# Kernel tuning notes

Hardware: AMD Instinct MI355X
Metric: run time of the kernel (lower is better)

Reference implementation:

```python
import jax, jax.numpy as jnp
import numpy as np

N_NODES = 50000
N_EDGES = 800000
F_IN = 128
HEADS = 4
C_OUT = 32
NEG_SLOPE = 0.2
BN_EPS = 1e-5


def _add_self_loops(edge_index, edge_attr, n):
    # PyG fill_value='mean': self-loop attr = mean of incoming edge attrs per node (0 if none)
    src, dst = edge_index[0], edge_index[1]
    deg = jax.ops.segment_sum(jnp.ones_like(edge_attr[:, 0]), dst, num_segments=n)
    loop_attr = jax.ops.segment_sum(edge_attr, dst, num_segments=n) / jnp.maximum(deg, 1.0)[:, None]
    loop = jnp.arange(n)
    src2 = jnp.concatenate([src, loop])
    dst2 = jnp.concatenate([dst, loop])
    attr2 = jnp.concatenate([edge_attr, loop_attr], axis=0)
    return src2, dst2, attr2


def _segment_softmax(logits, seg, n):
    m = jax.ops.segment_max(logits, seg, num_segments=n)
    m = jnp.where(jnp.isfinite(m), m, 0.0)
    ex = jnp.exp(logits - m[seg])
    s = jax.ops.segment_sum(ex, seg, num_segments=n)
    return ex / s[seg]


def _gatv2(x, src, dst, eattr, Wl, bl, Wr, br, We, att, bias, n):
    # x: [n, F]; returns [n, HEADS*C_OUT]
    xl = (x @ Wl + bl).reshape(n, HEADS, C_OUT)
    xr = (x @ Wr + br).reshape(n, HEADS, C_OUT)
    ea = (eattr @ We).reshape(-1, HEADS, C_OUT)
    xlj = xl[src]                                   # [E, H, C] gather
    msg = jax.nn.leaky_relu(xlj + xr[dst] + ea, NEG_SLOPE)
    logits = jnp.einsum('ehc,hc->eh', msg, att)     # [E, H]
    alpha = _segment_softmax(logits, dst, n)
    out = jax.ops.segment_sum(xlj * alpha[..., None], dst, num_segments=n)
    return out.reshape(n, HEADS * C_OUT) + bias


def _batchnorm(x, gamma, beta):
    mu = x.mean(axis=0)
    var = x.var(axis=0)
    return gamma * (x - mu) * jax.lax.rsqrt(var + BN_EPS) + beta


def setup_inputs() -> dict:
    key = jax.random.key(0)
    ks = jax.random.split(key, 20)
    HC = HEADS * C_OUT
    s = 0.05
    inp = {
        'emb': jax.random.normal(ks[0], (N_NODES, F_IN), dtype=jnp.float32),
        'edge_index': jax.random.randint(ks[1], (2, N_EDGES), 0, N_NODES, dtype=jnp.int64),
        'edge_weight': jax.random.uniform(ks[2], (N_EDGES, 1), dtype=jnp.float32),
        'Wl1': jax.random.normal(ks[3], (F_IN, HC)) * s,
        'bl1': jnp.zeros((HC,), jnp.float32),
        'Wr1': jax.random.normal(ks[4], (F_IN, HC)) * s,
        'br1': jnp.zeros((HC,), jnp.float32),
        'We1': jax.random.normal(ks[5], (1, HC)) * s,
        'att1': jax.random.normal(ks[6], (HEADS, C_OUT)) * s,
        'bias1': jnp.zeros((HC,), jnp.float32),
        'gamma1': jnp.ones((HC,), jnp.float32),
        'beta1': jnp.zeros((HC,), jnp.float32),
        'Wl2': jax.random.normal(ks[7], (HC, HC)) * s,
        'bl2': jnp.zeros((HC,), jnp.float32),
        'Wr2': jax.random.normal(ks[8], (HC, HC)) * s,
        'br2': jnp.zeros((HC,), jnp.float32),
        'We2': jax.random.normal(ks[9], (1, HC)) * s,
        'att2': jax.random.normal(ks[10], (HEADS, C_OUT)) * s,
        'bias2': jnp.zeros((HC,), jnp.float32),
    }
    return inp


def reference(emb, edge_index, edge_weight, Wl1, bl1, Wr1, br1, We1, att1, bias1,
              gamma1, beta1, Wl2, bl2, Wr2, br2, We2, att2, bias2):
    n = emb.shape[0]
    src, dst, eattr = _add_self_loops(edge_index, edge_weight, n)
    h1 = _gatv2(emb, src, dst, eattr, Wl1, bl1, Wr1, br1, We1, att1, bias1, n)
    h1 = jax.nn.elu(_batchnorm(h1, gamma1, beta1))
    h2 = _gatv2(h1, src, dst, eattr, Wl2, bl2, Wr2, br2, We2, att2, bias2, n)
    # fusion: mean over [input_emb, h1, h2] along stacked axis
    return (emb + h1 + h2) / 3.0
```

## Files before the change

kernel.cpp:

```cpp
#include <hip/hip_runtime.h>
#include <hip/hip_bf16.h>
#include <math.h>

#define N_NODES 50000
#define N_EDGES 800000
#define HC 128
#define SLOT 64

#define BM 128
#define NBX ((N_NODES + BM - 1) / BM)
#define NCHK 64
#define EPB (N_EDGES / NCHK)
#define NRNG 4
#define RNG_N (N_NODES / NRNG)
#define RNG_W (RNG_N / 2)
#define NW (N_NODES / 2)
#define NSCAT (NCHK * NRNG)
#define NB2 ((NW + 255) / 256)

typedef short bh8 __attribute__((ext_vector_type(8)));
typedef float f4 __attribute__((ext_vector_type(4)));
typedef float f2 __attribute__((ext_vector_type(2)));

__device__ __forceinline__ unsigned int pk2(float a, float b) {
  return (unsigned int)__bfloat16_as_ushort(__float2bfloat16(a)) |
         ((unsigned int)__bfloat16_as_ushort(__float2bfloat16(b)) << 16);
}
__device__ __forceinline__ float blo(unsigned int u) { return __uint_as_float(u << 16); }
__device__ __forceinline__ float bhi(unsigned int u) { return __uint_as_float(u & 0xffff0000u); }
__device__ __forceinline__ f2 vmax2(f2 a, f2 b) {
#if __has_builtin(__builtin_elementwise_max)
  return __builtin_elementwise_max(a, b);
#else
  f2 r; r.x = fmaxf(a.x, b.x); r.y = fmaxf(a.y, b.y); return r;
#endif
}

__global__ __launch_bounds__(256) void k_histprep(
    const float* __restrict__ Wl1, const float* __restrict__ Wr1,
    const float* __restrict__ Wl2, const float* __restrict__ Wr2,
    unsigned short* __restrict__ WtAll,
    float* __restrict__ chsum, float* __restrict__ chsq,
    const int* __restrict__ ei, unsigned int* __restrict__ counts32,
    int* __restrict__ done) {
  __shared__ unsigned int hist[RNG_W];
  int tid = threadIdx.x, bid = blockIdx.x;
  int gid = bid * 256 + tid;
  {
    int m = gid >> 14;
    int idx = gid & 16383;
    const float* src = (m == 0) ? Wl1 : (m == 1) ? Wr1 : (m == 2) ? Wl2 : Wr2;
    int k = idx >> 7, n = idx & 127;
    WtAll[((size_t)m * HC + n) * HC + k] =
        __bfloat16_as_ushort(__float2bfloat16(src[k * HC + n]));
    if (gid < HC) { chsum[gid] = 0.f; chsq[gid] = 0.f; }
    if (gid == 256) *done = 0;
  }
  int c = bid >> 2, r = bid & 3;
  int rb = r * RNG_N;
  for (int w = tid; w < RNG_W; w += 256) hist[w] = 0u;
  __syncthreads();
  const int* dstp = ei + N_EDGES + c * EPB;
  for (int g = tid; g < EPB / 4; g += 256) {
    int4 d4 = *(const int4*)(dstp + g * 4);
    int dl;
    dl = d4.x - rb; if ((unsigned)dl < RNG_N) atomicAdd(&hist[dl >> 1], (dl & 1) ? 0x10000u : 1u);
    dl = d4.y - rb; if ((unsigned)dl < RNG_N) atomicAdd(&hist[dl >> 1], (dl & 1) ? 0x10000u : 1u);
    dl = d4.z - rb; if ((unsigned)dl < RNG_N) atomicAdd(&hist[dl >> 1], (dl & 1) ? 0x10000u : 1u);
    dl = d4.w - rb; if ((unsigned)dl < RNG_N) atomicAdd(&hist[dl >> 1], (dl & 1) ? 0x10000u : 1u);
  }
  __syncthreads();
  unsigned int* dst = counts32 + (size_t)c * NW + r * RNG_W;
  for (int w = tid; w < RNG_W; w += 256) dst[w] = hist[w];
}

__global__ __launch_bounds__(256) void k_scan(const unsigned int* __restrict__ counts32,
                                              unsigned int* __restrict__ bases32,
                                              int* __restrict__ cursor,
                                              int* __restrict__ counts2,
                                              int* __restrict__ bases2,
                                              int* __restrict__ done) {
  __shared__ int dh[80];
  int tid = threadIdx.x;
  int w = blockIdx.x * 256 + tid;
  if (tid < 80) dh[tid] = 0;
  __syncthreads();
  if (w < NW) {
    unsigned int a0 = 0, a1 = 0;
#pragma unroll 4
    for (int b = 0; b < NCHK; ++b) {
      unsigned int v = counts32[(size_t)b * NW + w];
      bases32[(size_t)b * NW + w] = a0 | (a1 << 16);
      a0 += v & 0xffffu;
      a1 += v >> 16;
    }
    cursor[2 * w] = (int)a0;
    cursor[2 * w + 1] = (int)a1;
    atomicAdd(&dh[min((int)a0, SLOT)], 1);
    atomicAdd(&dh[min((int)a1, SLOT)], 1);
  }
  __syncthreads();
  if (tid <= SLOT) counts2[blockIdx.x * 72 + tid] = dh[tid];
  __threadfence();
  __shared__ int ticket;
  if (tid == 0) ticket = atomicAdd(done, 1);
  __syncthreads();
  if (ticket == NB2 - 1) {
    __threadfence();
    __shared__ int colsum[80], cbase[80];
    if (tid <= SLOT) {
      int s = 0;
      for (int b = 0; b < NB2; ++b) s += counts2[b * 72 + tid];
      colsum[tid] = s;
    }
    __syncthreads();
    if (tid == 0) {
      int a = 0;
      for (int i = 0; i <= SLOT; ++i) { cbase[i] = a; a += colsum[i]; }
    }
    __syncthreads();
    if (tid <= SLOT) {
      int a = cbase[tid];
      for (int b = 0; b < NB2; ++b) { bases2[b * 72 + tid] = a; a += counts2[b * 72 + tid]; }
    }
  }
}

__global__ __launch_bounds__(256) void k_scat_g1(
    const int* __restrict__ ei, const float* __restrict__ ew,
    const unsigned int* __restrict__ bases32, unsigned int* __restrict__ slots,
    const float* __restrict__ X, const unsigned short* __restrict__ Wt,
    const float* __restrict__ b0, const float* __restrict__ b1,
    unsigned short* __restrict__ Y0b, float* __restrict__ Y1,
    const int* __restrict__ cursor, const int* __restrict__ bases2,
    int* __restrict__ perm) {
  __shared__ __align__(16) unsigned int lsbuf[16384];
  int tid = threadIdx.x, bid = blockIdx.x;
  if (bid >= NSCAT + NBX) {
    int b2 = bid - NSCAT - NBX;
    int* dcur = (int*)lsbuf;
    if (tid <= SLOT) dcur[tid] = bases2[b2 * 72 + tid];
    __syncthreads();
    for (int i = tid; i < 512; i += 256) {
      int nn = b2 * 512 + i;
      if (nn < N_NODES) {
        int d = min(cursor[nn], SLOT);
        int pos = atomicAdd(&dcur[d], 1);
        perm[pos] = nn;
      }
    }
    return;
  }
  if (bid < NSCAT) {
    int c = bid >> 2, r = bid & 3;
    int rb = r * RNG_N;
    const unsigned int* bp = bases32 + (size_t)c * NW + r * RNG_W;
    for (int w = tid; w < RNG_W; w += 256) lsbuf[w] = bp[w];
    __syncthreads();
    const int* sp = ei + c * EPB;
    const int* dp = ei + N_EDGES + c * EPB;
    const float* wp = ew + c * EPB;
    for (int g = tid; g < EPB / 4; g += 256) {
      int4 s4 = *(const int4*)(sp + g * 4);
      int4 d4 = *(const int4*)(dp + g * 4);
      float4 w4 = *(const float4*)(wp + g * 4);
      int ss[4] = {s4.x, s4.y, s4.z, s4.w};
      int dd[4] = {d4.x, d4.y, d4.z, d4.w};
      float ww[4] = {w4.x, w4.y, w4.z, w4.w};
#pragma unroll
      for (int i = 0; i < 4; ++i) {
        int dl = dd[i] - rb;
        if ((unsigned)dl < RNG_N) {
          unsigned int old = atomicAdd(&lsbuf[dl >> 1], (dl & 1) ? 0x10000u : 1u);
          unsigned int pos = (dl & 1) ? (old >> 16) : (old & 0xffffu);
          unsigned int wq = min((unsigned int)(ww[i] * 65536.f + 0.5f), 65535u);
          if (pos < SLOT)
            slots[(size_t)dd[i] * SLOT + pos] = ((unsigned int)ss[i] << 16) | wq;
        }
      }
    }
    return;
  }
  unsigned short* Xls = (unsigned short*)lsbuf;
  unsigned short* Wls = Xls + 128 * 128;
  int row0 = (bid - NSCAT) * BM;
  {
    int r = tid >> 1;
    int ks = (tid & 1) * 64;
    int gr = row0 + r;
    const float* xp = X + (size_t)gr * HC + ks;
    int sw = r & 15;
#pragma unroll
    for (int i = 0; i < 4; ++i) {
      float f[16];
      if (gr < N_NODES) {
        *(float4*)&f[0] = *(const float4*)(xp + i * 16);
        *(float4*)&f[4] = *(const float4*)(xp + i * 16 + 4);
        *(float4*)&f[8] = *(const float4*)(xp + i * 16 + 8);
        *(float4*)&f[12] = *(const float4*)(xp + i * 16 + 12);
      } else {
#pragma unroll
        for (int j = 0; j < 16; ++j) f[j] = 0.f;
      }
      int kg = (ks >> 3) + i * 2;
      *(uint4*)&Xls[r * 128 + ((kg ^ sw) * 8)] =
          make_uint4(pk2(f[0], f[1]), pk2(f[2], f[3]), pk2(f[4], f[5]), pk2(f[6], f[7]));
      *(uint4*)&Xls[r * 128 + (((kg + 1) ^ sw) * 8)] =
          make_uint4(pk2(f[8], f[9]), pk2(f[10], f[11]), pk2(f[12], f[13]), pk2(f[14], f[15]));
    }
  }
  int lane = tid & 63;
  int wv = tid >> 6;
  int lrow = lane & 15;
  int lq = lane >> 4;
  int rbase = wv * 32;
#pragma unroll
  for (int half = 0; half < 2; ++half) {
    if (half) __syncthreads();
    {
      int n = tid >> 1;
      int ks2 = (tid & 1) * 64;
      const unsigned short* wp = Wt + half * (HC * HC) + n * HC + ks2;
      int swn = n & 15;
#pragma unroll
      for (int g = 0; g < 8; ++g) {
        uint4 v = *(const uint4*)(wp + g * 8);
        int kg = (ks2 >> 3) + g;
        *(uint4*)&Wls[n * 128 + ((kg ^ swn) * 8)] = v;
      }
    }
    __syncthreads();
    f4 acc[2][8];
#pragma unroll
    for (int mt = 0; mt < 2; ++mt)
#pragma unroll
      for (int nt = 0; nt < 8; ++nt) acc[mt][nt] = (f4){0.f, 0.f, 0.f, 0.f};
#pragma unroll
    for (int kk = 0; kk < 4; ++kk) {
      int kg = kk * 4 + lq;
      bh8 a0 = *(const bh8*)&Xls[(rbase + lrow) * 128 + ((kg ^ lrow) * 8)];
      bh8 a1 = *(const bh8*)&Xls[(rbase + 16 + lrow) * 128 + ((kg ^ lrow) * 8)];
#pragma unroll
      for (int nt = 0; nt < 8; ++nt) {
        bh8 b = *(const bh8*)&Wls[(nt * 16 + lrow) * 128 + ((kg ^ lrow) * 8)];
        acc[0][nt] = __builtin_amdgcn_mfma_f32_16x16x32_bf16(a0, b, acc[0][nt], 0, 0, 0);
        acc[1][nt] = __builtin_amdgcn_mfma_f32_16x16x32_bf16(a1, b, acc[1][nt], 0, 0, 0);
      }
    }
    const float* bb = half ? b1 : b0;
    float bv[8];
#pragma unroll
    for (int nt = 0; nt < 8; ++nt) bv[nt] = bb[nt * 16 + lrow];
#pragma unroll
    for (int mt = 0; mt < 2; ++mt) {
#pragma unroll
      for (int rr = 0; rr < 4; ++rr) {
        int gr = row0 + rbase + mt * 16 + lq * 4 + rr;
        if (gr < N_NODES) {
          if (half == 0) {
#pragma unroll
            for (int nt = 0; nt < 8; ++nt)
              Y0b[(size_t)gr * HC + nt * 16 + lrow] =
                  __bfloat16_as_ushort(__float2bfloat16(acc[mt][nt][rr] + bv[nt]));
          } else {
#pragma unroll
            for (int nt = 0; nt < 8; ++nt)
              Y1[(size_t)gr * HC + nt * 16 + lrow] = acc[mt][nt][rr] + bv[nt];
          }
        }
      }
    }
  }
}

__global__ __launch_bounds__(256) void k_gemm2(
    const unsigned short* __restrict__ Xb, const unsigned short* __restrict__ Wt,
    const float* __restrict__ b0, const float* __restrict__ b1,
    unsigned char* __restrict__ Y0f8, float* __restrict__ Y1,
    const float* __restrict__ chsum, const float* __restrict__ chsq,
    const float* __restrict__ gamma, const float* __restrict__ beta) {
  __shared__ __align__(16) unsigned short Xls[128 * 128];
  __shared__ __align__(16) unsigned short Wls[128 * 128];
  __shared__ float ssc[HC], ssh[HC];
  int tid = threadIdx.x;
  if (tid < HC) {
    float mu = chsum[tid] * (1.f / N_NODES);
    float var = chsq[tid] * (1.f / N_NODES) - mu * mu;
    float sc = gamma[tid] * rsqrtf(var + 1e-5f);
    ssc[tid] = sc;
    ssh[tid] = beta[tid] - mu * sc;
  }
  __syncthreads();
  int row0 = blockIdx.x * BM;
  {
    int r = tid >> 1;
    int ks = (tid & 1) * 64;
    int gr = row0 + r;
    const unsigned short* xp = Xb + (size_t)gr * HC + ks;
    int sw = r & 15;
#pragma unroll
    for (int i = 0; i < 4; ++i) {
      float f[16];
      if (gr < N_NODES) {
        uint4 ua = *(const uint4*)(xp + i * 16);
        uint4 ub = *(const uint4*)(xp + i * 16 + 8);
        f[0] = blo(ua.x); f[1] = bhi(ua.x); f[2] = blo(ua.y); f[3] = bhi(ua.y);
        f[4] = blo(ua.z); f[5] = bhi(ua.z); f[6] = blo(ua.w); f[7] = bhi(ua.w);
        f[8] = blo(ub.x); f[9] = bhi(ub.x); f[10] = blo(ub.y); f[11] = bhi(ub.y);
        f[12] = blo(ub.z); f[13] = bhi(ub.z); f[14] = blo(ub.w); f[15] = bhi(ub.w);
      } else {
#pragma unroll
        for (int j = 0; j < 16; ++j) f[j] = 0.f;
      }
#pragma unroll
      for (int j = 0; j < 16; ++j) {
        float y = fmaf(f[j], ssc[ks + i * 16 + j], ssh[ks + i * 16 + j]);
        f[j] = (y > 0.f) ? y : (__expf(y) - 1.f);
      }
      int kg = (ks >> 3) + i * 2;
      *(uint4*)&Xls[r * 128 + ((kg ^ sw) * 8)] =
          make_uint4(pk2(f[0], f[1]), pk2(f[2], f[3]), pk2(f[4], f[5]), pk2(f[6], f[7]));
      *(uint4*)&Xls[r * 128 + (((kg + 1) ^ sw) * 8)] =
          make_uint4(pk2(f[8], f[9]), pk2(f[10], f[11]), pk2(f[12], f[13]), pk2(f[14], f[15]));
    }
  }
  int lane = tid & 63;
  int wv = tid >> 6;
  int lrow = lane & 15;
  int lq = lane >> 4;
  int rbase = wv * 32;
#pragma unroll
  for (int half = 0; half < 2; ++half) {
    if (half) __syncthreads();
    {
      int n = tid >> 1;
      int ks = (tid & 1) * 64;
      const unsigned short* wp = Wt + half * (HC * HC) + n * HC + ks;
      int swn = n & 15;
#pragma unroll
      for (int g = 0; g < 8; ++g) {
        uint4 v = *(const uint4*)(wp + g * 8);
        int kg = (ks >> 3) + g;
        *(uint4*)&Wls[n * 128 + ((kg ^ swn) * 8)] = v;
      }
    }
    __syncthreads();
    f4 acc[2][8];
#pragma unroll
    for (int mt = 0; mt < 2; ++mt)
#pragma unroll
      for (int nt = 0; nt < 8; ++nt) acc[mt][nt] = (f4){0.f, 0.f, 0.f, 0.f};
#pragma unroll
    for (int kk = 0; kk < 4; ++kk) {
      int kg = kk * 4 + lq;
      bh8 a0 = *(const bh8*)&Xls[(rbase + lrow) * 128 + ((kg ^ lrow) * 8)];
      bh8 a1 = *(const bh8*)&Xls[(rbase + 16 + lrow) * 128 + ((kg ^ lrow) * 8)];
#pragma unroll
      for (int nt = 0; nt < 8; ++nt) {
        bh8 b = *(const bh8*)&Wls[(nt * 16 + lrow) * 128 + ((kg ^ lrow) * 8)];
        acc[0][nt] = __builtin_amdgcn_mfma_f32_16x16x32_bf16(a0, b, acc[0][nt], 0, 0, 0);
        acc[1][nt] = __builtin_amdgcn_mfma_f32_16x16x32_bf16(a1, b, acc[1][nt], 0, 0, 0);
      }
    }
    const float* bb = half ? b1 : b0;
    float bv[8];
#pragma unroll
    for (int nt = 0; nt < 8; ++nt) bv[nt] = bb[nt * 16 + lrow];
#pragma unroll
    for (int mt = 0; mt < 2; ++mt) {
#pragma unroll
      for (int rr = 0; rr < 4; ++rr) {
        int gr = row0 + rbase + mt * 16 + lq * 4 + rr;
        if (gr < N_NODES) {
          if (half == 0) {
#pragma unroll
            for (int nt = 0; nt < 8; ++nt) {
              float v = acc[mt][nt][rr] + bv[nt];
              int p = __builtin_amdgcn_cvt_pk_fp8_f32(v, v, 0, false);
              Y0f8[(size_t)gr * HC + nt * 16 + lrow] = (unsigned char)(p & 0xff);
            }
          } else {
#pragma unroll
            for (int nt = 0; nt < 8; ++nt)
              Y1[(size_t)gr * HC + nt * 16 + lrow] = acc[mt][nt][rr] + bv[nt];
          }
        }
      }
    }
  }
}

template <int FINAL, int F8>
__global__ __launch_bounds__(256) void k_gat(
    const void* __restrict__ xlv, const float* __restrict__ xr,
    const int* __restrict__ cursor, const unsigned int* __restrict__ slots,
    const int* __restrict__ perm,
    const float* __restrict__ We, const float* __restrict__ att,
    const float* __restrict__ bias, void* __restrict__ out,
    const float* __restrict__ emb, const unsigned short* __restrict__ h1p,
    const float* __restrict__ chsum, const float* __restrict__ chsq,
    const float* __restrict__ gamma, const float* __restrict__ beta) {
  int g = threadIdx.x >> 4;
  int lane = threadIdx.x & 15;
  int n = perm[blockIdx.x * 16 + g];
  int ci = lane * 2;
  int fr = n * 32 + ci;
  const uint4* xl4 = (const uint4*)xlv;
  const uint2* xf2 = (const uint2*)xlv;
  float4 xa = ((const float4*)xr)[fr], xb = ((const float4*)xr)[fr + 1];
  float4 wa = ((const float4*)We)[ci], wb = ((const float4*)We)[ci + 1];
  float4 aa = ((const float4*)att)[ci], ab = ((const float4*)att)[ci + 1];
  const float LOG2E = 1.4426950408889634f;
  const float WSC = 1.f / 65536.f;
  f2 xr01 = {xa.x, xa.y}, xr23 = {xa.z, xa.w}, xr45 = {xb.x, xb.y}, xr67 = {xb.z, xb.w};
  f2 we01 = {wa.x * WSC, wa.y * WSC}, we23 = {wa.z * WSC, wa.w * WSC};
  f2 we45 = {wb.x * WSC, wb.y * WSC}, we67 = {wb.z * WSC, wb.w * WSC};
  f2 at01 = {aa.x * LOG2E, aa.y * LOG2E}, at23 = {aa.z * LOG2E, aa.w * LOG2E};
  f2 at45 = {ab.x * LOG2E, ab.y * LOG2E}, at67 = {ab.z * LOG2E, ab.w * LOG2E};
  int deg = min(cursor[n], SLOT);
  int base = n * SLOT;
  int deg32 = min(deg, 32);

  unsigned int ev0 = (lane < deg32) ? slots[base + lane] : 0u;
  unsigned int ev1 = (16 + lane < deg32) ? slots[base + 16 + lane] : 0u;
  float wsum = (float)(ev0 & 0xffffu) + (float)(ev1 & 0xffffu);
#pragma unroll
  for (int m = 8; m >= 1; m >>= 1) wsum += __shfl_xor(wsum, m);

  float l = 0.f;
  f2 o01 = {0.f, 0.f}, o23 = {0.f, 0.f}, o45 = {0.f, 0.f}, o67 = {0.f, 0.f};

  auto edge_body = [&](float w, uint4 q, bool valid) {
    f2 a0, a1, a2, a3;
    if (F8) {
      a0 = __builtin_amdgcn_cvt_pk_f32_fp8((int)q.x, false);
      a1 = __builtin_amdgcn_cvt_pk_f32_fp8((int)q.x, true);
      a2 = __builtin_amdgcn_cvt_pk_f32_fp8((int)q.y, false);
      a3 = __builtin_amdgcn_cvt_pk_f32_fp8((int)q.y, true);
    } else {
      a0 = (f2){blo(q.x), bhi(q.x)};
      a1 = (f2){blo(q.y), bhi(q.y)};
      a2 = (f2){blo(q.z), bhi(q.z)};
      a3 = (f2){blo(q.w), bhi(q.w)};
    }
    f2 m0 = (a0 + xr01) + w * we01;
    f2 m1 = (a1 + xr23) + w * we23;
    f2 m2 = (a2 + xr45) + w * we45;
    f2 m3 = (a3 + xr67) + w * we67;
    m0 = vmax2(m0, m0 * 0.2f);
    m1 = vmax2(m1, m1 * 0.2f);
    m2 = vmax2(m2, m2 * 0.2f);
    m3 = vmax2(m3, m3 * 0.2f);
    f2 t = m0 * at01 + m1 * at23;
    t = t + (m2 * at45 + m3 * at67);
    float p = t.x + t.y;
    p += __shfl_xor(p, 1);
    p += __shfl_xor(p, 2);
#if __has_builtin(__builtin_amdgcn_exp2f)
    float e = valid ? __builtin_amdgcn_exp2f(p) : 0.f;
#else
    float e = valid ? __expf(p * 0.6931471805599453f) : 0.f;
#endif
    l += e;
    o01 = o01 + e * a0;
    o23 = o23 + e * a1;
    o45 = o45 + e * a2;
    o67 = o67 + e * a3;
  };
  auto fetch = [&](int j, uint4& q, float& w) {
    int jc = min(j, deg32 - 1);
    unsigned int evs = (jc & 16) ? ev1 : ev0;
    unsigned int evj = __shfl(evs, jc & 15, 16);
    w = (float)(evj & 0xffffu);
    int s = (int)(evj >> 16);
    if (F8) { uint2 t = xf2[s * 16 + lane]; q.x = t.x; q.y = t.y; }
    else q = xl4[s * 16 + lane];
  };

  if (deg32 > 0) {
    uint4 q0, q1;
    float w0, w1;
    fetch(0, q0, w0);
    fetch(1, q1, w1);
    for (int b = 0; b < deg32; b += 2) {
      edge_body(w0, q0, true);
      fetch(b + 2, q0, w0);
      edge_body(w1, q1, b + 1 < deg32);
      fetch(b + 3, q1, w1);
    }
  }
  if (deg > 32) {
    for (int j = base + 32; j < base + deg; ++j) {
      unsigned int evj = slots[j];
      float w = (float)(evj & 0xffffu);
      wsum += w;
      int s = (int)(evj >> 16);
      uint4 gc;
      if (F8) { uint2 t = xf2[s * 16 + lane]; gc.x = t.x; gc.y = t.y; }
      else gc = xl4[s * 16 + lane];
      edge_body(w, gc, true);
    }
  }
  {
    float wself = (deg > 0) ? wsum / (float)deg : 0.f;
    uint4 gs;
    if (F8) { uint2 t = xf2[n * 16 + lane]; gs.x = t.x; gs.y = t.y; }
    else gs = xl4[n * 16 + lane];
    edge_body(wself, gs, true);
  }

  float inv = 1.f / l;
  float4 ba = ((const float4*)bias)[ci], bbv = ((const float4*)bias)[ci + 1];
  float r0 = fmaf(o01.x, inv, ba.x), r1 = fmaf(o01.y, inv, ba.y);
  float r2 = fmaf(o23.x, inv, ba.z), r3 = fmaf(o23.y, inv, ba.w);
  float r4 = fmaf(o45.x, inv, bbv.x), r5 = fmaf(o45.y, inv, bbv.y);
  float r6 = fmaf(o67.x, inv, bbv.z), r7 = fmaf(o67.y, inv, bbv.w);
  if (FINAL) {
    float4 ea = ((const float4*)emb)[fr], eb = ((const float4*)emb)[fr + 1];
    uint4 hh = ((const uint4*)h1p)[n * 16 + lane];
    float hv[8] = {blo(hh.x), bhi(hh.x), blo(hh.y), bhi(hh.y),
                   blo(hh.z), bhi(hh.z), blo(hh.w), bhi(hh.w)};
    float4 csa = ((const float4*)chsum)[ci], csb = ((const float4*)chsum)[ci + 1];
    float4 cqa = ((const float4*)chsq)[ci], cqb = ((const float4*)chsq)[ci + 1];
    float4 gma = ((const float4*)gamma)[ci], gmb = ((const float4*)gamma)[ci + 1];
    float4 bta = ((const float4*)beta)[ci], btb = ((const float4*)beta)[ci + 1];
    float cs[8] = {csa.x, csa.y, csa.z, csa.w, csb.x, csb.y, csb.z, csb.w};
    float cq[8] = {cqa.x, cqa.y, cqa.z, cqa.w, cqb.x, cqb.y, cqb.z, cqb.w};
    float gm[8] = {gma.x, gma.y, gma.z, gma.w, gmb.x, gmb.y, gmb.z, gmb.w};
    float bt[8] = {bta.x, bta.y, bta.z, bta.w, btb.x, btb.y, btb.z, btb.w};
    float ev4[8] = {ea.x, ea.y, ea.z, ea.w, eb.x, eb.y, eb.z, eb.w};
    float rr[8] = {r0, r1, r2, r3, r4, r5, r6, r7};
    const float invN = 1.f / N_NODES;
    const float k3 = 1.f / 3.f;
#pragma unroll
    for (int k = 0; k < 8; ++k) {
      float mu = cs[k] * invN;
      float var = cq[k] * invN - mu * mu;
      float sc = gm[k] * rsqrtf(var + 1e-5f);
      float sh = bt[k] - mu * sc;
      float h = fmaf(hv[k], sc, sh);
      h = (h > 0.f) ? h : (__expf(h) - 1.f);
      rr[k] = (ev4[k] + h + rr[k]) * k3;
    }
    ((float4*)out)[fr] = make_float4(rr[0], rr[1], rr[2], rr[3]);
    ((float4*)out)[fr + 1] = make_float4(rr[4], rr[5], rr[6], rr[7]);
  } else {
    ((uint4*)out)[n * 16 + lane] =
        make_uint4(pk2(r0, r1), pk2(r2, r3), pk2(r4, r5), pk2(r6, r7));
  }
}

#define BN_ROWS 200
__global__ __launch_bounds__(256) void k_bnstats(const unsigned short* __restrict__ h1b,
                                                 float* __restrict__ chsum,
                                                 float* __restrict__ chsq) {
  int c2 = threadIdx.x & 63;
  int g = threadIdx.x >> 6;
  int r0 = blockIdx.x * BN_ROWS;
  float s0 = 0.f, s1 = 0.f, q0 = 0.f, q1 = 0.f;
  const unsigned int* h32 = (const unsigned int*)h1b;
  for (int r = r0 + g; r < r0 + BN_ROWS; r += 4) {
    unsigned int u = h32[(size_t)r * 64 + c2];
    float a = blo(u), b = bhi(u);
    s0 += a; q0 += a * a;
    s1 += b; q1 += b * b;
  }
  __shared__ float sh[256][4];
  sh[threadIdx.x][0] = s0; sh[threadIdx.x][1] = q0;
  sh[threadIdx.x][2] = s1; sh[threadIdx.x][3] = q1;
  __syncthreads();
  if (g == 0) {
    float ts0 = 0.f, tq0 = 0.f, ts1 = 0.f, tq1 = 0.f;
#pragma unroll
    for (int gg = 0; gg < 4; ++gg) {
      ts0 += sh[gg * 64 + c2][0]; tq0 += sh[gg * 64 + c2][1];
      ts1 += sh[gg * 64 + c2][2]; tq1 += sh[gg * 64 + c2][3];
    }
    atomicAdd(chsum + 2 * c2, ts0);
    atomicAdd(chsq + 2 * c2, tq0);
    atomicAdd(chsum + 2 * c2 + 1, ts1);
    atomicAdd(chsq + 2 * c2 + 1, tq1);
  }
}

extern "C" void kernel_launch(void* const* d_in, const int* in_sizes, int n_in,
                              void* d_out, int out_size, void* d_ws, size_t ws_size,
                              hipStream_t stream) {
  const float* emb = (const float*)d_in[0];
  const int* ei = (const int*)d_in[1];
  const float* ew = (const float*)d_in[2];
  const float* Wl1 = (const float*)d_in[3];
  const float* bl1 = (const float*)d_in[4];
  const float* Wr1 = (const float*)d_in[5];
  const float* br1 = (const float*)d_in[6];
  const float* We1 = (const float*)d_in[7];
  const float* att1 = (const float*)d_in[8];
  const float* bias1 = (const float*)d_in[9];
  const float* gamma1 = (const float*)d_in[10];
  const float* beta1 = (const float*)d_in[11];
  const float* Wl2 = (const float*)d_in[12];
  const float* bl2 = (const float*)d_in[13];
  const float* Wr2 = (const float*)d_in[14];
  const float* br2 = (const float*)d_in[15];
  const float* We2 = (const float*)d_in[16];
  const float* att2 = (const float*)d_in[17];
  const float* bias2 = (const float*)d_in[18];
  float* out = (float*)d_out;

  char* wsb = (char*)d_ws;
  size_t off = 0;
  auto alloc = [&](size_t bytes) -> void* {
    void* p = (void*)(wsb + off);
    off += (bytes + 255) & ~(size_t)255;
    return p;
  };
  int* cursor = (int*)alloc((size_t)N_NODES * 4);
  float* chsum = (float*)alloc(HC * 4);
  float* chsq = (float*)alloc(HC * 4);
  unsigned short* WtAll = (unsigned short*)alloc((size_t)4 * HC * HC * 2);
  unsigned int* counts32 = (unsigned int*)alloc((size_t)NCHK * NW * 4);
  unsigned int* bases32 = (unsigned int*)alloc((size_t)NCHK * NW * 4);
  unsigned int* slots = (unsigned int*)alloc((size_t)N_NODES * SLOT * 4);
  unsigned short* xlb = (unsigned short*)alloc((size_t)N_NODES * HC * 2);
  unsigned char* xlf8 = (unsigned char*)alloc((size_t)N_NODES * HC);
  float* xr = (float*)alloc((size_t)N_NODES * HC * 4);
  unsigned short* h1b = (unsigned short*)alloc((size_t)N_NODES * HC * 2);
  int* counts2 = (int*)alloc((size_t)NB2 * 72 * 4);
  int* bases2 = (int*)alloc((size_t)NB2 * 72 * 4);
  int* perm = (int*)alloc((size_t)N_NODES * 4);
  int* done = (int*)alloc(256);

  k_histprep<<<NSCAT, 256, 0, stream>>>(Wl1, Wr1, Wl2, Wr2, WtAll, chsum, chsq,
                                        ei, counts32, done);
  k_scan<<<NB2, 256, 0, stream>>>(counts32, bases32, cursor, counts2, bases2, done);
  k_scat_g1<<<NSCAT + NBX + NB2, 256, 0, stream>>>(ei, ew, bases32, slots, emb,
                                                   WtAll, bl1, br1, xlb, xr,
                                                   cursor, bases2, perm);
  k_gat<0, 0><<<N_NODES / 16, 256, 0, stream>>>(xlb, xr, cursor, slots, perm, We1,
                                                att1, bias1, (void*)h1b, nullptr,
                                                nullptr, nullptr, nullptr, nullptr,
                                                nullptr);
  k_bnstats<<<N_NODES / BN_ROWS, 256, 0, stream>>>(h1b, chsum, chsq);
  k_gemm2<<<NBX, 256, 0, stream>>>(h1b, WtAll + 2 * HC * HC, bl2, br2, xlf8, xr,
                                   chsum, chsq, gamma1, beta1);
  k_gat<1, 1><<<N_NODES / 16, 256, 0, stream>>>(xlf8, xr, cursor, slots, perm, We2,
                                                att2, bias2, (void*)out, emb, h1b,
                                                chsum, chsq, gamma1, beta1);
}
```

Baseline: 281.9 us.

## Fuse BN statistics into layer-1 GAT kernel, deepen edge prefetch, reverse node order

Removes the separate batch-norm statistics kernel. The layer-1 GAT kernel now reduces per-channel sum and sum-of-squares itself, using wave shuffles, shared-memory atomics and one global atomic per channel per block. The edge loop now keeps three gathers in flight instead of two, and blocks walk the degree-sorted permutation in reverse. This saves a kernel launch and a full re-read of h1, at the cost of extra shuffles, shared atomics and a __syncthreads in the GAT kernel, plus more registers for the deeper prefetch.

Result: slower. 312.0 us (+10.7%).

```diff
diff --git a/kernel.cpp b/kernel.cpp
--- a/kernel.cpp
+++ b/kernel.cpp
@@ -398,11 +398,16 @@
     const float* __restrict__ We, const float* __restrict__ att,
     const float* __restrict__ bias, void* __restrict__ out,
     const float* __restrict__ emb, const unsigned short* __restrict__ h1p,
-    const float* __restrict__ chsum, const float* __restrict__ chsq,
+    float* __restrict__ chsum, float* __restrict__ chsq,
     const float* __restrict__ gamma, const float* __restrict__ beta) {
+  __shared__ float ssum[HC], ssq[HC];
   int g = threadIdx.x >> 4;
   int lane = threadIdx.x & 15;
-  int n = perm[blockIdx.x * 16 + g];
+  if (!FINAL) {
+    if (threadIdx.x < HC) { ssum[threadIdx.x] = 0.f; ssq[threadIdx.x] = 0.f; }
+    __syncthreads();
+  }
+  int n = perm[(N_NODES - 1) - (blockIdx.x * 16 + g)];
   int ci = lane * 2;
   int fr = n * 32 + ci;
   const uint4* xl4 = (const uint4*)xlv;
@@ -478,15 +483,18 @@
   };
 
   if (deg32 > 0) {
-    uint4 q0, q1;
-    float w0, w1;
+    uint4 q0, q1, q2;
+    float w0, w1, w2;
     fetch(0, q0, w0);
     fetch(1, q1, w1);
-    for (int b = 0; b < deg32; b += 2) {
+    fetch(2, q2, w2);
+    for (int b = 0; b < deg32; b += 3) {
       edge_body(w0, q0, true);
-      fetch(b + 2, q0, w0);
+      fetch(b + 3, q0, w0);
       edge_body(w1, q1, b + 1 < deg32);
-      fetch(b + 3, q1, w1);
+      fetch(b + 4, q1, w1);
+      edge_body(w2, q2, b + 2 < deg32);
+      fetch(b + 5, q2, w2);
     }
   }
   if (deg > 32) {
@@ -545,41 +553,26 @@
     ((float4*)out)[fr] = make_float4(rr[0], rr[1], rr[2], rr[3]);
     ((float4*)out)[fr + 1] = make_float4(rr[4], rr[5], rr[6], rr[7]);
   } else {
-    ((uint4*)out)[n * 16 + lane] =
-        make_uint4(pk2(r0, r1), pk2(r2, r3), pk2(r4, r5), pk2(r6, r7));
-  }
-}
-
-#define BN_ROWS 200
-__global__ __launch_bounds__(256) void k_bnstats(const unsigned short* __restrict__ h1b,
-                                                 float* __restrict__ chsum,
-                                                 float* __restrict__ chsq) {
-  int c2 = threadIdx.x & 63;
-  int g = threadIdx.x >> 6;
-  int r0 = blockIdx.x * BN_ROWS;
-  float s0 = 0.f, s1 = 0.f, q0 = 0.f, q1 = 0.f;
-  const unsigned int* h32 = (const unsigned int*)h1b;
-  for (int r = r0 + g; r < r0 + BN_ROWS; r += 4) {
-    unsigned int u = h32[(size_t)r * 64 + c2];
-    float a = blo(u), b = bhi(u);
-    s0 += a; q0 += a * a;
-    s1 += b; q1 += b * b;
-  }
-  __shared__ float sh[256][4];
-  sh[threadIdx.x][0] = s0; sh[threadIdx.x][1] = q0;
-  sh[threadIdx.x][2] = s1; sh[threadIdx.x][3] = q1;
-  __syncthreads();
-  if (g == 0) {
-    float ts0 = 0.f, tq0 = 0.f, ts1 = 0.f, tq1 = 0.f;
-#pragma unroll
-    for (int gg = 0; gg < 4; ++gg) {
-      ts0 += sh[gg * 64 + c2][0]; tq0 += sh[gg * 64 + c2][1];
-      ts1 += sh[gg * 64 + c2][2]; tq1 += sh[gg * 64 + c2][3];
-    }
-    atomicAdd(chsum + 2 * c2, ts0);
-    atomicAdd(chsq + 2 * c2, tq0);
-    atomicAdd(chsum + 2 * c2 + 1, ts1);
-    atomicAdd(chsq + 2 * c2 + 1, tq1);
+    uint4 pkv = make_uint4(pk2(r0, r1), pk2(r2, r3), pk2(r4, r5), pk2(r6, r7));
+    ((uint4*)out)[n * 16 + lane] = pkv;
+    float hv[8] = {blo(pkv.x), bhi(pkv.x), blo(pkv.y), bhi(pkv.y),
+                   blo(pkv.z), bhi(pkv.z), blo(pkv.w), bhi(pkv.w)};
+#pragma unroll
+    for (int k = 0; k < 8; ++k) {
+      float s = hv[k];
+      float q = hv[k] * hv[k];
+      s += __shfl_xor(s, 16); s += __shfl_xor(s, 32);
+      q += __shfl_xor(q, 16); q += __shfl_xor(q, 32);
+      if ((threadIdx.x & 48) == 0) {
+        atomicAdd(&ssum[lane * 8 + k], s);
+        atomicAdd(&ssq[lane * 8 + k], q);
+      }
+    }
+    __syncthreads();
+    if (threadIdx.x < HC) {
+      atomicAdd(chsum + threadIdx.x, ssum[threadIdx.x]);
+      atomicAdd(chsq + threadIdx.x, ssq[threadIdx.x]);
+    }
   }
 }
 
@@ -638,9 +631,8 @@
                                                    cursor, bases2, perm);
   k_gat<0, 0><<<N_NODES / 16, 256, 0, stream>>>(xlb, xr, cursor, slots, perm, We1,
                                                 att1, bias1, (void*)h1b, nullptr,
-                                                nullptr, nullptr, nullptr, nullptr,
+                                                nullptr, chsum, chsq, nullptr,
                                                 nullptr);
-  k_bnstats<<<N_NODES / BN_ROWS, 256, 0, stream>>>(h1b, chsum, chsq);
   k_gemm2<<<NBX, 256, 0, stream>>>(h1b, WtAll + 2 * HC * HC, bl2, br2, xlf8, xr,
                                    chsum, chsq, gamma1, beta1);
   k_gat<1, 1><<<N_NODES / 16, 256, 0, stream>>>(xlf8, xr, cursor, slots, perm, We2,
```
